# Kernel optimization log

Hardware: AMD Instinct MI355X
Metric: run time of the kernel (lower is better)

The kernel has to match this reference:

```python
import jax, jax.numpy as jnp
import numpy as np

# ---- model hyperparams (match init_kwargs / Mamba1 defaults) ----
SEQ_LEN, PRED_LEN, PATCH, STRIDE = 512, 96, 16, 16
D_MODEL, N_LAYER, N_VARS = 128, 2, 32
D_INNER, D_STATE, D_CONV, DT_RANK = 2 * D_MODEL, 16, 4, 8  # d_inner=2*d_model, dt_rank=ceil(d_model/16)
BATCH = 16
EPS = 1e-5


def setup_inputs() -> dict:
    key = jax.random.key(0)
    ks = jax.random.split(key, 20)
    s = 0.02
    inp = {
        'x_enc': jax.random.normal(ks[0], (BATCH, SEQ_LEN, N_VARS), jnp.float32),
        'x_mark_enc': jax.random.normal(ks[1], (BATCH, SEQ_LEN, 4), jnp.float32),
        'x_dec': jax.random.normal(ks[2], (BATCH, PRED_LEN, N_VARS), jnp.float32),
        'x_mark_dec': jax.random.normal(ks[3], (BATCH, PRED_LEN, 4), jnp.float32),
        # patch embedding: Linear(patch_len -> d_model, bias=False)
        'patch_w': jax.random.normal(ks[4], (D_MODEL, PATCH), jnp.float32) * s,
        # per-layer Mamba1 params, stacked on leading layer axis
        'norm_w': jnp.ones((N_LAYER, D_MODEL), jnp.float32),
        'in_proj_w': jax.random.normal(ks[5], (N_LAYER, 2 * D_INNER, D_MODEL), jnp.float32) * s,
        'conv_w': jax.random.normal(ks[6], (N_LAYER, D_INNER, D_CONV), jnp.float32) * s,
        'conv_b': jnp.zeros((N_LAYER, D_INNER), jnp.float32),
        'x_proj_w': jax.random.normal(ks[7], (N_LAYER, DT_RANK + 2 * D_STATE, D_INNER), jnp.float32) * s,
        'dt_proj_w': jax.random.normal(ks[8], (N_LAYER, D_INNER, DT_RANK), jnp.float32) * s,
        'dt_proj_b': jax.random.normal(ks[9], (N_LAYER, D_INNER), jnp.float32) * 0.1 - 4.0,  # softplus -> small dt
        'A_log': jnp.tile(jnp.log(jnp.arange(1, D_STATE + 1, dtype=jnp.float32))[None, None, :], (N_LAYER, D_INNER, 1)),
        'D_skip': jnp.ones((N_LAYER, D_INNER), jnp.float32),
        'out_proj_w': jax.random.normal(ks[10], (N_LAYER, D_MODEL, D_INNER), jnp.float32) * s,
        'final_norm_w': jnp.ones((D_MODEL,), jnp.float32),
        # head: Linear(d_model*seq_len//patch_len -> pred_len)
        'head_w': jax.random.normal(ks[11], (PRED_LEN, D_MODEL * SEQ_LEN // PATCH), jnp.float32) * s,
        'head_b': jnp.zeros((PRED_LEN,), jnp.float32),
    }
    return inp


def rmsnorm(x, w):
    return x * jax.lax.rsqrt(jnp.mean(x * x, axis=-1, keepdims=True) + EPS) * w


def selective_scan(u, dt, A, Bm, Cm, Dp):
    # u, dt: (B,L,Di); Bm, Cm: (B,L,N); A: (Di,N); Dp: (Di,)
    def step(h, inp):
        dt_t, B_t, C_t, u_t = inp  # (B,Di),(B,N),(B,N),(B,Di)
        dA = jnp.exp(dt_t[:, :, None] * A)                      # (B,Di,N)
        h = dA * h + dt_t[:, :, None] * B_t[:, None, :] * u_t[:, :, None]
        y = jnp.einsum('bdn,bn->bd', h, C_t)
        return h, y

    B_, L, Di = u.shape
    h0 = jnp.zeros((B_, Di, A.shape[1]), u.dtype)
    xs = (dt.transpose(1, 0, 2), Bm.transpose(1, 0, 2), Cm.transpose(1, 0, 2), u.transpose(1, 0, 2))
    _, ys = jax.lax.scan(step, h0, xs)
    return ys.transpose(1, 0, 2) + u * Dp  # skip connection D*u


def mamba_mixer(x, in_w, cw, cb, xp_w, dt_w, dt_b, A_log, Dp, out_w):
    # x: (B,L,d_model)
    xz = x @ in_w.T                                   # (B,L,2*Di)
    xs_, z = jnp.split(xz, 2, axis=-1)
    xc = xs_.transpose(0, 2, 1)                       # (B,Di,L)
    xc = jax.lax.conv_general_dilated(
        xc, cw[:, None, :], (1,), [(D_CONV - 1, 0)],  # causal depthwise conv
        dimension_numbers=('NCH', 'OIH', 'NCH'), feature_group_count=D_INNER)
    xc = jax.nn.silu(xc + cb[None, :, None])
    u = xc.transpose(0, 2, 1)                         # (B,L,Di)
    x_dbl = u @ xp_w.T                                # (B,L,dt_rank+2N)
    dt, Bm, Cm = jnp.split(x_dbl, [DT_RANK, DT_RANK + D_STATE], axis=-1)
    dt = jax.nn.softplus(dt @ dt_w.T + dt_b)          # (B,L,Di)
    A = -jnp.exp(A_log)                               # (Di,N)
    y = selective_scan(u, dt, A, Bm, Cm, Dp)
    y = y * jax.nn.silu(z)
    return y @ out_w.T


def reference(x_enc, x_mark_enc, x_dec, x_mark_dec, patch_w, norm_w, in_proj_w,
              conv_w, conv_b, x_proj_w, dt_proj_w, dt_proj_b, A_log, D_skip,
              out_proj_w, final_norm_w, head_w, head_b):
    b, _, c = x_enc.shape
    # instance norm over time (stats detached)
    means = jax.lax.stop_gradient(jnp.mean(x_enc, axis=1, keepdims=True))
    xe = x_enc - means
    stdev = jax.lax.stop_gradient(jnp.sqrt(jnp.var(xe, axis=1, keepdims=True) + EPS))
    xe = xe / stdev
    # patching: stride == patch_len so unfold == reshape
    xp = xe.transpose(0, 2, 1).reshape(b, c, SEQ_LEN // PATCH, PATCH)  # (b,c,l,patch)
    enc = jnp.einsum('bclp,dp->bcld', xp, patch_w).reshape(b, c * (SEQ_LEN // PATCH), D_MODEL)
    # Mamba encoder: pre-norm residual blocks + final norm
    x = enc
    for i in range(N_LAYER):
        h = rmsnorm(x, norm_w[i])
        x = x + mamba_mixer(h, in_proj_w[i], conv_w[i], conv_b[i], x_proj_w[i],
                            dt_proj_w[i], dt_proj_b[i], A_log[i], D_skip[i], out_proj_w[i])
    x = rmsnorm(x, final_norm_w)
    # prediction head: b (c l) d -> (b c) (l d) -> linear -> (b, pred, c)
    l = SEQ_LEN // PATCH
    xh = x.reshape(b, c, l * D_MODEL)
    out = xh @ head_w.T + head_b                      # (b,c,pred)
    dec_out = out.transpose(0, 2, 1)                  # (b,pred,c)
    dec_out = dec_out * stdev[:, :1, :] + means[:, :1, :]
    return dec_out
```

## Files before the change

### kernel.cpp

```cpp
#include <hip/hip_runtime.h>
#include <hip/hip_bf16.h>
#include <math.h>

#define BATCH   16
#define SEQL    512
#define NVARS   32
#define PATCHL  16
#define LTOK    32
#define DMODEL  128
#define NLAYER  2
#define DIN     256
#define DSTATE  16
#define DTRANK  8
#define DCONV   4
#define PRED    96
#define TOK     1024
#define NTOK    (BATCH*TOK)
#define EPSF    1e-5f
#define NCH     64
#define CHL     16

typedef __attribute__((ext_vector_type(8))) short bf16x8;
typedef __attribute__((ext_vector_type(4))) float f32x4;
typedef __hip_bfloat16 bf16;

__global__ __launch_bounds__(256) void k_cast(
    const float* __restrict__ a, const float* __restrict__ b,
    const float* __restrict__ c, const float* __restrict__ d,
    int na, int nb, int nc, int nd, bf16* __restrict__ out,
    const float* __restrict__ A_log, float* __restrict__ a1s, int* __restrict__ pwf,
    float* __restrict__ hg)
{
    int i = blockIdx.x * 256 + threadIdx.x;
    int total = na + nb + nc + nd;
    if (i < total) {
        float v;
        if (i < na) v = a[i];
        else if (i < na + nb) v = b[i - na];
        else if (i < na + nb + nc) v = c[i - na - nb];
        else v = d[i - na - nb - nc];
        out[i] = __float2bfloat16(v);
    } else if (i < total + NLAYER * DIN) {
        int j = i - total;
        const float* al = A_log + (size_t)j * DSTATE;
        float a1 = -__expf(al[0]);
        bool pw = true;
        #pragma unroll
        for (int n = 1; n < 16; n++) {
            float av = -__expf(al[n]);
            pw = pw && (fabsf(av - (n + 1) * a1) <= 1e-5f * fabsf((n + 1) * a1));
        }
        a1s[j] = a1;
        pwf[j] = pw ? 1 : 0;
    } else if (i < total + NLAYER * DIN + 512 * PRED) {
        hg[i - total - NLAYER * DIN] = 0.f;
    }
}

__global__ __launch_bounds__(256) void k_instnorm_patch(
    const float* __restrict__ x_enc, const float* __restrict__ patch_w,
    const float* __restrict__ nw0,
    float* __restrict__ x, bf16* __restrict__ hbf,
    float* __restrict__ means, float* __restrict__ stdev)
{
    int bc = blockIdx.x;
    int b = bc >> 5, c = bc & 31;
    __shared__ float xe[SEQL];
    __shared__ float pw[DMODEL * PATCHL];
    __shared__ float red[8];
    __shared__ float enc_lds[LTOK][DMODEL];
    int tid = threadIdx.x;

    float v0 = x_enc[((size_t)b * SEQL + tid) * NVARS + c];
    float v1 = x_enc[((size_t)b * SEQL + tid + 256) * NVARS + c];
    for (int i = tid; i < DMODEL * PATCHL; i += 256) pw[i] = patch_w[i];

    float s = v0 + v1;
    for (int o = 1; o < 64; o <<= 1) s += __shfl_xor(s, o, 64);
    if ((tid & 63) == 0) red[tid >> 6] = s;
    __syncthreads();
    float mean = (red[0] + red[1] + red[2] + red[3]) * (1.f / 512.f);

    float d0 = v0 - mean, d1 = v1 - mean;
    float q = d0 * d0 + d1 * d1;
    for (int o = 1; o < 64; o <<= 1) q += __shfl_xor(q, o, 64);
    if ((tid & 63) == 0) red[4 + (tid >> 6)] = q;
    __syncthreads();
    float var = (red[4] + red[5] + red[6] + red[7]) * (1.f / 512.f);
    float sd = sqrtf(var + EPSF);
    float rsd = 1.f / sd;
    if (tid == 0) { means[bc] = mean; stdev[bc] = sd; }

    xe[tid] = d0 * rsd;
    xe[tid + 256] = d1 * rsd;
    __syncthreads();

    size_t base = ((size_t)b * TOK + (size_t)c * LTOK) * DMODEL;
    for (int o = tid; o < LTOK * DMODEL; o += 256) {
        int l = o >> 7, dm = o & 127;
        float acc = 0.f;
        #pragma unroll
        for (int p = 0; p < PATCHL; p++) acc += xe[l * PATCHL + p] * pw[dm * PATCHL + p];
        x[base + o] = acc;
        enc_lds[l][dm] = acc;
    }
    __syncthreads();

    int t = tid >> 3, g = tid & 7;
    float vals[16];
    float ss = 0.f;
    #pragma unroll
    for (int j = 0; j < 16; j++) { vals[j] = enc_lds[t][g * 16 + j]; ss += vals[j] * vals[j]; }
    ss += __shfl_xor(ss, 1, 64);
    ss += __shfl_xor(ss, 2, 64);
    ss += __shfl_xor(ss, 4, 64);
    float rms = rsqrtf(ss * (1.f / DMODEL) + EPSF);
    bf16* hp = hbf + (base + (size_t)t * DMODEL);
    #pragma unroll
    for (int j = 0; j < 16; j++)
        hp[g * 16 + j] = __float2bfloat16(vals[j] * rms * nw0[g * 16 + j]);
}

template <int MODE>
__global__ __launch_bounds__(256) void mfma_gemm(
    const bf16* __restrict__ A, const bf16* __restrict__ W,
    float* __restrict__ C, bf16* __restrict__ C2, bf16* __restrict__ C3,
    int M, int N, int K, int lda, int kper)
{
    __shared__ ushort Asm[128][40];
    __shared__ ushort Wsm[128][40];
    int bm = blockIdx.y * 128, bn = blockIdx.x * 128;
    int tid = threadIdx.x;
    int w = tid >> 6, l = tid & 63;
    int wr = w >> 1, wc = w & 1;
    int kb = (l >> 4) * 8, lr = l & 15;

    f32x4 acc[4][4];
    #pragma unroll
    for (int i = 0; i < 4; i++)
        #pragma unroll
        for (int j = 0; j < 4; j++) acc[i][j] = (f32x4){0.f, 0.f, 0.f, 0.f};

    int kbeg = blockIdx.z * kper;
    for (int k0 = kbeg; k0 < kbeg + kper; k0 += 32) {
        #pragma unroll
        for (int i = 0; i < 2; i++) {
            int idx = tid + 256 * i;
            int row = idx >> 2, kq = (idx & 3) * 8;
            *(float4*)&Asm[row][kq] =
                *(const float4*)&A[(size_t)(bm + row) * lda + k0 + kq];
            float4 wv = make_float4(0.f, 0.f, 0.f, 0.f);
            if (bn + row < N)
                wv = *(const float4*)&W[(size_t)(bn + row) * K + k0 + kq];
            *(float4*)&Wsm[row][kq] = wv;
        }
        __syncthreads();
        bf16x8 af[4], bfr[4];
        #pragma unroll
        for (int f = 0; f < 4; f++) {
            af[f]  = *(const bf16x8*)&Asm[wr * 64 + f * 16 + lr][kb];
            bfr[f] = *(const bf16x8*)&Wsm[wc * 64 + f * 16 + lr][kb];
        }
        #pragma unroll
        for (int mf = 0; mf < 4; mf++)
            #pragma unroll
            for (int nf = 0; nf < 4; nf++)
                acc[mf][nf] = __builtin_amdgcn_mfma_f32_16x16x32_bf16(
                    af[mf], bfr[nf], acc[mf][nf], 0, 0, 0);
        __syncthreads();
    }

    int rbase = bm + wr * 64 + (l >> 4) * 4;
    int cbase = bn + wc * 64 + lr;
    #pragma unroll
    for (int mf = 0; mf < 4; mf++) {
        #pragma unroll
        for (int nf = 0; nf < 4; nf++) {
            int n = cbase + nf * 16;
            if (n >= N) continue;
            #pragma unroll
            for (int r = 0; r < 4; r++) {
                int m = rbase + mf * 16 + r;
                float v = acc[mf][nf][r];
                if (MODE == 2) atomicAdd(&C[(size_t)m * N + n], v);
                else {
                    if (n < 256) C3[(size_t)m * 256 + n] = __float2bfloat16(v);
                    else C2[(size_t)m * 256 + (n - 256)] = __float2bfloat16(v);
                }
            }
        }
    }
}

__device__ __forceinline__ float softplus_f(float x) {
    return (x > 8.f) ? x : __logf(1.f + __expf(x));
}

__global__ __launch_bounds__(256) void k_convx1(
    const bf16* __restrict__ xs, const float* __restrict__ cw,
    const float* __restrict__ cb, const bf16* __restrict__ xw,
    const float* __restrict__ dtw, const float* __restrict__ dtb_,
    const float* __restrict__ a1s, const int* __restrict__ pwf,
    const float* __restrict__ A_log,
    bf16* __restrict__ ubf, float* __restrict__ xdbl,
    bf16* __restrict__ q, float* __restrict__ sdt_out)
{
    int blk = blockIdx.x;
    int b = blk >> 6, ch = blk & (NCH - 1);
    int d = threadIdx.x;
    __shared__ ushort u_lds[16][264];
    __shared__ float xdbl_lds[16][40];

    float c0 = cw[d * 4], c1 = cw[d * 4 + 1], c2 = cw[d * 4 + 2], c3 = cw[d * 4 + 3];
    float cbias = cb[d];
    int tloc0 = ch * CHL;
    const bf16* col = xs + ((size_t)b * TOK + tloc0) * 256 + d;
    float xv[19];
    #pragma unroll
    for (int i = 0; i < 19; i++) {
        int tg = tloc0 - 3 + i;
        xv[i] = (tg >= 0) ? __bfloat162float(col[(size_t)(i - 3) * 256]) : 0.f;
    }
    bf16* uout = ubf + ((size_t)b * TOK + tloc0) * 256 + d;
    #pragma unroll
    for (int t = 0; t < 16; t++) {
        float a = cbias + xv[t] * c0 + xv[t + 1] * c1 + xv[t + 2] * c2 + xv[t + 3] * c3;
        float s = __fdividef(a, 1.f + __expf(-a));
        bf16 ub = __float2bfloat16(s);
        u_lds[t][d] = *(ushort*)&ub;
        uout[(size_t)t * 256] = ub;
    }
    __syncthreads();

    int w = d >> 6, l = d & 63;
    if (w < 3) {
        int lr = l & 15, kb = (l >> 4) * 8;
        int nrow = w * 16 + lr;
        bool valid = nrow < 40;
        const bf16* wrow = xw + (size_t)nrow * 256;
        f32x4 acc = (f32x4){0.f, 0.f, 0.f, 0.f};
        #pragma unroll
        for (int ks = 0; ks < 8; ks++) {
            bf16x8 af = *(const bf16x8*)&u_lds[lr][ks * 32 + kb];
            bf16x8 bfr = (bf16x8){0, 0, 0, 0, 0, 0, 0, 0};
            if (valid) bfr = *(const bf16x8*)&wrow[ks * 32 + kb];
            acc = __builtin_amdgcn_mfma_f32_16x16x32_bf16(af, bfr, acc, 0, 0, 0);
        }
        int ncol = w * 16 + (l & 15);
        if (ncol < 40) {
            #pragma unroll
            for (int r = 0; r < 4; r++) {
                int t = (l >> 4) * 4 + r;
                xdbl_lds[t][ncol] = acc[r];
                xdbl[((size_t)b * TOK + tloc0 + t) * 40 + ncol] = acc[r];
            }
        }
    }
    __syncthreads();

    float a1 = a1s[d];
    bool pw = pwf[d] != 0;
    float w8[8];
    #pragma unroll
    for (int j = 0; j < 8; j++) w8[j] = dtw[d * 8 + j];
    float bias = dtb_[d];
    float h[16];
    #pragma unroll
    for (int n = 0; n < 16; n++) h[n] = 0.f;
    float sdt = 0.f;

    if (pw) {
        for (int t = 0; t < CHL; t++) {
            float acc = bias;
            #pragma unroll
            for (int j = 0; j < 8; j++) acc += xdbl_lds[t][j] * w8[j];
            float dtv = softplus_f(acc);
            ushort uraw = u_lds[t][d];
            float uu = __bfloat162float(*(bf16*)&uraw);
            sdt += dtv;
            float du = dtv * uu;
            float dA[16];
            dA[0] = __expf(dtv * a1);
            #pragma unroll
            for (int n = 1; n < 16; n++) dA[n] = dA[(n - 1) >> 1] * dA[n >> 1];
            #pragma unroll
            for (int n = 0; n < 16; n++)
                h[n] = dA[n] * h[n] + du * xdbl_lds[t][8 + n];
        }
    } else {
        float Av[16];
        #pragma unroll
        for (int n = 0; n < 16; n++) Av[n] = -__expf(A_log[d * 16 + n]);
        for (int t = 0; t < CHL; t++) {
            float acc = bias;
            #pragma unroll
            for (int j = 0; j < 8; j++) acc += xdbl_lds[t][j] * w8[j];
            float dtv = softplus_f(acc);
            ushort uraw = u_lds[t][d];
            float uu = __bfloat162float(*(bf16*)&uraw);
            sdt += dtv;
            float du = dtv * uu;
            #pragma unroll
            for (int n = 0; n < 16; n++)
                h[n] = __expf(dtv * Av[n]) * h[n] + du * xdbl_lds[t][8 + n];
        }
    }
    bf16* qp = q + ((size_t)blk * 16) * 256 + d;
    #pragma unroll
    for (int n = 0; n < 16; n++) qp[(size_t)n * 256] = __float2bfloat16(h[n]);
    sdt_out[(size_t)blk * 256 + d] = sdt;
}

__global__ __launch_bounds__(256) void k_scan2(
    const float* __restrict__ A_log, const float* __restrict__ sdt_in,
    bf16* __restrict__ q)
{
    int idx = blockIdx.x * 256 + threadIdx.x;
    int d = idx & 255, n = (idx >> 8) & 15, b = idx >> 12;
    float Av = -__expf(A_log[d * 16 + n]);
    float h = 0.f;
    for (int g = 0; g < NCH / 8; g++) {
        float qv[8], sv[8];
        #pragma unroll
        for (int j = 0; j < 8; j++) {
            size_t blk = (size_t)b * NCH + g * 8 + j;
            qv[j] = __bfloat162float(q[(blk * 16 + n) * 256 + d]);
            sv[j] = sdt_in[blk * 256 + d];
        }
        #pragma unroll
        for (int j = 0; j < 8; j++) {
            size_t blk = (size_t)b * NCH + g * 8 + j;
            float P = __expf(Av * sv[j]);
            q[(blk * 16 + n) * 256 + d] = __float2bfloat16(h);
            h = P * h + qv[j];
        }
    }
}

__global__ __launch_bounds__(256) void k_scan3o(
    const bf16* __restrict__ ubf, const float* __restrict__ xdbl,
    const float* __restrict__ dtw, const float* __restrict__ dtb_,
    const float* __restrict__ a1s, const int* __restrict__ pwf,
    const float* __restrict__ A_log, const float* __restrict__ Dp,
    const bf16* __restrict__ q, const bf16* __restrict__ zbf,
    const bf16* __restrict__ ow, const float* __restrict__ nwn,
    float* __restrict__ x, bf16* __restrict__ hout)
{
    int blk = blockIdx.x;
    int b = blk >> 6, ch = blk & (NCH - 1);
    int d = threadIdx.x;
    __shared__ ushort y_lds[16][264];
    __shared__ float xn_lds[16][132];

    float a1 = a1s[d];
    bool pw = pwf[d] != 0;
    float w8[8];
    #pragma unroll
    for (int j = 0; j < 8; j++) w8[j] = dtw[d * 8 + j];
    float bias = dtb_[d];
    float Dv = Dp[d];
    float h[16];
    const bf16* qp = q + ((size_t)blk * 16) * 256 + d;
    #pragma unroll
    for (int n = 0; n < 16; n++) h[n] = __bfloat162float(qp[(size_t)n * 256]);

    size_t tok0 = (size_t)b * TOK + ch * CHL;
    const float* row = xdbl + tok0 * 40;
    const bf16* up = ubf + tok0 * 256 + d;
    const bf16* zp = zbf + tok0 * 256 + d;

    if (pw) {
        for (int t = 0; t < CHL; t++, row += 40, up += 256, zp += 256) {
            float acc = bias;
            #pragma unroll
            for (int j = 0; j < 8; j++) acc += row[j] * w8[j];
            float dtv = softplus_f(acc);
            float uu = __bfloat162float(*up);
            float du = dtv * uu;
            float dA[16];
            dA[0] = __expf(dtv * a1);
            #pragma unroll
            for (int n = 1; n < 16; n++) dA[n] = dA[(n - 1) >> 1] * dA[n >> 1];
            float ya = 0.f;
            #pragma unroll
            for (int n = 0; n < 16; n++) {
                h[n] = dA[n] * h[n] + du * row[8 + n];
                ya += h[n] * row[24 + n];
            }
            float zv = __bfloat162float(*zp);
            float sz = __fdividef(zv, 1.f + __expf(-zv));
            bf16 yb = __float2bfloat16((ya + uu * Dv) * sz);
            y_lds[t][d] = *(ushort*)&yb;
        }
    } else {
        float Av[16];
        #pragma unroll
        for (int n = 0; n < 16; n++) Av[n] = -__expf(A_log[d * 16 + n]);
        for (int t = 0; t < CHL; t++, row += 40, up += 256, zp += 256) {
            float acc = bias;
            #pragma unroll
            for (int j = 0; j < 8; j++) acc += row[j] * w8[j];
            float dtv = softplus_f(acc);
            float uu = __bfloat162float(*up);
            float du = dtv * uu;
            float ya = 0.f;
            #pragma unroll
            for (int n = 0; n < 16; n++) {
                h[n] = __expf(dtv * Av[n]) * h[n] + du * row[8 + n];
                ya += h[n] * row[24 + n];
            }
            float zv = __bfloat162float(*zp);
            float sz = __fdividef(zv, 1.f + __expf(-zv));
            bf16 yb = __float2bfloat16((ya + uu * Dv) * sz);
            y_lds[t][d] = *(ushort*)&yb;
        }
    }
    __syncthreads();

    int w = d >> 6, l = d & 63;
    int lr = l & 15, kb = (l >> 4) * 8;
    const bf16* wr0 = ow + (size_t)(w * 32 + lr) * 256;
    const bf16* wr1 = ow + (size_t)(w * 32 + 16 + lr) * 256;
    f32x4 acc0 = (f32x4){0.f, 0.f, 0.f, 0.f};
    f32x4 acc1 = (f32x4){0.f, 0.f, 0.f, 0.f};
    #pragma unroll
    for (int ks = 0; ks < 8; ks++) {
        bf16x8 af = *(const bf16x8*)&y_lds[lr][ks * 32 + kb];
        bf16x8 b0 = *(const bf16x8*)&wr0[ks * 32 + kb];
        bf16x8 b1 = *(const bf16x8*)&wr1[ks * 32 + kb];
        acc0 = __builtin_amdgcn_mfma_f32_16x16x32_bf16(af, b0, acc0, 0, 0, 0);
        acc1 = __builtin_amdgcn_mfma_f32_16x16x32_bf16(af, b1, acc1, 0, 0, 0);
    }
    int trow = (l >> 4) * 4;
    float* xp = x + (tok0 + trow) * (size_t)DMODEL;
    #pragma unroll
    for (int r = 0; r < 4; r++) {
        float v0 = xp[(size_t)r * DMODEL + w * 32 + lr] + acc0[r];
        float v1 = xp[(size_t)r * DMODEL + w * 32 + 16 + lr] + acc1[r];
        xp[(size_t)r * DMODEL + w * 32 + lr] = v0;
        xp[(size_t)r * DMODEL + w * 32 + 16 + lr] = v1;
        xn_lds[trow + r][w * 32 + lr] = v0;
        xn_lds[trow + r][w * 32 + 16 + lr] = v1;
    }
    __syncthreads();

    int t = d >> 4, g = d & 15;
    float vals[8];
    float ss = 0.f;
    #pragma unroll
    for (int j = 0; j < 8; j++) { vals[j] = xn_lds[t][g * 8 + j]; ss += vals[j] * vals[j]; }
    ss += __shfl_xor(ss, 1, 64);
    ss += __shfl_xor(ss, 2, 64);
    ss += __shfl_xor(ss, 4, 64);
    ss += __shfl_xor(ss, 8, 64);
    float rms = rsqrtf(ss * (1.f / DMODEL) + EPSF);
    bf16* hp = hout + (tok0 + t) * (size_t)DMODEL;
    #pragma unroll
    for (int j = 0; j < 8; j++)
        hp[g * 8 + j] = __float2bfloat16(vals[j] * rms * nwn[g * 8 + j]);
}

__global__ __launch_bounds__(256) void k_head_ep(
    const float* __restrict__ hg, const float* __restrict__ hb,
    const float* __restrict__ means, const float* __restrict__ stdev,
    float* __restrict__ out)
{
    int i = blockIdx.x * 256 + threadIdx.x;
    if (i >= BATCH * PRED * NVARS) return;
    int c = i & 31;
    int p = (i >> 5) % PRED;
    int b = i / (PRED * NVARS);
    float v = hg[((size_t)b * NVARS + c) * PRED + p] + hb[p];
    out[i] = v * stdev[b * NVARS + c] + means[b * NVARS + c];
}

extern "C" void kernel_launch(void* const* d_in, const int* in_sizes, int n_in,
                              void* d_out, int out_size, void* d_ws, size_t ws_size,
                              hipStream_t stream)
{
    const float* x_enc   = (const float*)d_in[0];
    const float* patch_w = (const float*)d_in[4];
    const float* norm_w  = (const float*)d_in[5];
    const float* in_w    = (const float*)d_in[6];
    const float* conv_w  = (const float*)d_in[7];
    const float* conv_b  = (const float*)d_in[8];
    const float* xp_w    = (const float*)d_in[9];
    const float* dt_w    = (const float*)d_in[10];
    const float* dt_b    = (const float*)d_in[11];
    const float* A_log   = (const float*)d_in[12];
    const float* D_skip  = (const float*)d_in[13];
    const float* out_w   = (const float*)d_in[14];
    const float* fnorm_w = (const float*)d_in[15];
    const float* head_w  = (const float*)d_in[16];
    const float* head_b  = (const float*)d_in[17];
    float* out = (float*)d_out;

    float* ws    = (float*)d_ws;
    float* means = ws;
    float* stdv  = ws + 512;
    float* x     = ws + 1024;
    float* xdbl  = x    + (size_t)NTOK * 128;
    float* sbuf  = xdbl + (size_t)NTOK * 40;
    float* hg    = sbuf + (size_t)BATCH * NCH * DIN;
    float* a1s   = hg + 512 * PRED;
    int*   pwf   = (int*)(a1s + NLAYER * DIN);
    bf16* hbf  = (bf16*)(pwf + NLAYER * DIN);
    bf16* xsbf = hbf + (size_t)NTOK * 128;
    bf16* zbf  = xsbf + (size_t)NTOK * 256;
    bf16* ubf  = zbf + (size_t)NTOK * 256;
    bf16* qbuf = ubf + (size_t)NTOK * 256;
    bf16* wbf  = qbuf + (size_t)BATCH * NCH * DSTATE * DIN;

    const int NIW = NLAYER * 2 * DIN * DMODEL;
    const int NXW = NLAYER * (DTRANK + 2*DSTATE) * DIN;
    const int NOW = NLAYER * DMODEL * DIN;
    const int NHW = PRED * LTOK * DMODEL;
    bf16* iwbf = wbf;
    bf16* xwbf = iwbf + NIW;
    bf16* owbf = xwbf + NXW;
    bf16* hwbf = owbf + NOW;

    int castN = NIW + NXW + NOW + NHW + NLAYER * DIN + 512 * PRED;
    k_cast<<<(castN + 255) / 256, 256, 0, stream>>>(
        in_w, xp_w, out_w, head_w, NIW, NXW, NOW, NHW, wbf, A_log, a1s, pwf, hg);

    k_instnorm_patch<<<BATCH * NVARS, 256, 0, stream>>>(
        x_enc, patch_w, norm_w, x, hbf, means, stdv);

    for (int layer = 0; layer < NLAYER; layer++) {
        const float* cw  = conv_w + layer * DIN * DCONV;
        const float* cb  = conv_b + layer * DIN;
        const float* dw  = dt_w   + layer * DIN * DTRANK;
        const float* db  = dt_b   + layer * DIN;
        const float* al  = A_log  + layer * DIN * DSTATE;
        const float* dp  = D_skip + layer * DIN;
        const float* a1l = a1s + layer * DIN;
        const int*   pwl = pwf + layer * DIN;
        const bf16* iw = iwbf + (size_t)layer * 2 * DIN * DMODEL;
        const bf16* xw = xwbf + (size_t)layer * (DTRANK + 2 * DSTATE) * DIN;
        const bf16* ow = owbf + (size_t)layer * DMODEL * DIN;
        const float* nwn = (layer + 1 < NLAYER) ? (norm_w + (layer + 1) * DMODEL) : fnorm_w;

        mfma_gemm<3><<<dim3(4, NTOK / 128, 1), 256, 0, stream>>>(
            hbf, iw, nullptr, zbf, xsbf, NTOK, 512, DMODEL, DMODEL, DMODEL);
        k_convx1<<<BATCH * NCH, 256, 0, stream>>>(
            xsbf, cw, cb, xw, dw, db, a1l, pwl, al, ubf, xdbl, qbuf, sbuf);
        k_scan2<<<(BATCH * DIN * DSTATE) / 256, 256, 0, stream>>>(al, sbuf, qbuf);
        k_scan3o<<<BATCH * NCH, 256, 0, stream>>>(
            ubf, xdbl, dw, db, a1l, pwl, al, dp, qbuf, zbf, ow, nwn, x, hbf);
    }

    mfma_gemm<2><<<dim3(1, 4, 32), 256, 0, stream>>>(
        hbf, hwbf, hg, nullptr, nullptr, 512, PRED, LTOK * DMODEL, LTOK * DMODEL, 128);
    k_head_ep<<<(BATCH * PRED * NVARS + 255) / 256, 256, 0, stream>>>(
        hg, head_b, means, stdv, out);
}
```

Measured before the change: 156.4 us.

## Fuse in_proj GEMM into conv and scan-output kernels

Removes the standalone in_proj GEMM per layer. The x-half projection is now computed inside k_convx1 over a 32-token window, the last 16 tokens of the previous chunk supplying the conv halo. The z-half is computed inside k_scan3o from hbf before hbf is overwritten. This drops two bf16 NTOK×256 intermediate buffers and one launch per layer, at the cost of recomputing halo rows, extra LDS, and weight loads repeated per block from global or L2.

After: 155.0 us. Within noise of the previous version (-0.9%).

```diff
diff --git a/kernel.cpp b/kernel.cpp
--- a/kernel.cpp
+++ b/kernel.cpp
@@ -121,11 +121,9 @@
         hp[g * 16 + j] = __float2bfloat16(vals[j] * rms * nw0[g * 16 + j]);
 }
 
-template <int MODE>
-__global__ __launch_bounds__(256) void mfma_gemm(
+__global__ __launch_bounds__(256) void mfma_gemm_at(
     const bf16* __restrict__ A, const bf16* __restrict__ W,
-    float* __restrict__ C, bf16* __restrict__ C2, bf16* __restrict__ C3,
-    int M, int N, int K, int lda, int kper)
+    float* __restrict__ C, int M, int N, int K, int kper)
 {
     __shared__ ushort Asm[128][40];
     __shared__ ushort Wsm[128][40];
@@ -148,7 +146,7 @@
             int idx = tid + 256 * i;
             int row = idx >> 2, kq = (idx & 3) * 8;
             *(float4*)&Asm[row][kq] =
-                *(const float4*)&A[(size_t)(bm + row) * lda + k0 + kq];
+                *(const float4*)&A[(size_t)(bm + row) * K + k0 + kq];
             float4 wv = make_float4(0.f, 0.f, 0.f, 0.f);
             if (bn + row < N)
                 wv = *(const float4*)&W[(size_t)(bn + row) * K + k0 + kq];
@@ -179,15 +177,8 @@
             int n = cbase + nf * 16;
             if (n >= N) continue;
             #pragma unroll
-            for (int r = 0; r < 4; r++) {
-                int m = rbase + mf * 16 + r;
-                float v = acc[mf][nf][r];
-                if (MODE == 2) atomicAdd(&C[(size_t)m * N + n], v);
-                else {
-                    if (n < 256) C3[(size_t)m * 256 + n] = __float2bfloat16(v);
-                    else C2[(size_t)m * 256 + (n - 256)] = __float2bfloat16(v);
-                }
-            }
+            for (int r = 0; r < 4; r++)
+                atomicAdd(&C[(size_t)(rbase + mf * 16 + r) * N + n], acc[mf][nf][r]);
         }
     }
 }
@@ -197,8 +188,9 @@
 }
 
 __global__ __launch_bounds__(256) void k_convx1(
-    const bf16* __restrict__ xs, const float* __restrict__ cw,
-    const float* __restrict__ cb, const bf16* __restrict__ xw,
+    const bf16* __restrict__ hbf, const bf16* __restrict__ iwA,
+    const float* __restrict__ cw, const float* __restrict__ cb,
+    const bf16* __restrict__ xw,
     const float* __restrict__ dtw, const float* __restrict__ dtb_,
     const float* __restrict__ a1s, const int* __restrict__ pwf,
     const float* __restrict__ A_log,
@@ -208,18 +200,69 @@
     int blk = blockIdx.x;
     int b = blk >> 6, ch = blk & (NCH - 1);
     int d = threadIdx.x;
+    __shared__ ushort hb_lds[32][136];
+    __shared__ ushort xs_lds[32][264];
     __shared__ ushort u_lds[16][264];
     __shared__ float xdbl_lds[16][40];
 
+    int tloc0 = ch * CHL;
+
+    {
+        int r = d >> 3, c8 = (d & 7) * 16;
+        int tl = tloc0 - 16 + r;
+        float4 v0 = make_float4(0.f, 0.f, 0.f, 0.f), v1 = v0;
+        if (tl >= 0) {
+            const bf16* src = hbf + ((size_t)b * TOK + tl) * DMODEL + c8;
+            v0 = *(const float4*)src;
+            v1 = *(const float4*)(src + 8);
+        }
+        *(float4*)&hb_lds[r][c8] = v0;
+        *(float4*)&hb_lds[r][c8 + 8] = v1;
+    }
+    __syncthreads();
+
+    {
+        int w = d >> 6, l = d & 63;
+        int lr = l & 15, kb = (l >> 4) * 8;
+        f32x4 accx[2][4];
+        #pragma unroll
+        for (int mf = 0; mf < 2; mf++)
+            #pragma unroll
+            for (int nf = 0; nf < 4; nf++) accx[mf][nf] = (f32x4){0.f, 0.f, 0.f, 0.f};
+        #pragma unroll
+        for (int ks = 0; ks < 4; ks++) {
+            bf16x8 af0 = *(const bf16x8*)&hb_lds[lr][ks * 32 + kb];
+            bf16x8 af1 = *(const bf16x8*)&hb_lds[16 + lr][ks * 32 + kb];
+            #pragma unroll
+            for (int nf = 0; nf < 4; nf++) {
+                const bf16* wrow = iwA + (size_t)(w * 64 + nf * 16 + lr) * DMODEL;
+                bf16x8 bfr = *(const bf16x8*)&wrow[ks * 32 + kb];
+                accx[0][nf] = __builtin_amdgcn_mfma_f32_16x16x32_bf16(af0, bfr, accx[0][nf], 0, 0, 0);
+                accx[1][nf] = __builtin_amdgcn_mfma_f32_16x16x32_bf16(af1, bfr, accx[1][nf], 0, 0, 0);
+            }
+        }
+        #pragma unroll
+        for (int mf = 0; mf < 2; mf++)
+            #pragma unroll
+            for (int nf = 0; nf < 4; nf++) {
+                int ncol = w * 64 + nf * 16 + lr;
+                #pragma unroll
+                for (int r = 0; r < 4; r++) {
+                    int row = mf * 16 + (l >> 4) * 4 + r;
+                    bf16 xb = __float2bfloat16(accx[mf][nf][r]);
+                    xs_lds[row][ncol] = *(ushort*)&xb;
+                }
+            }
+    }
+    __syncthreads();
+
     float c0 = cw[d * 4], c1 = cw[d * 4 + 1], c2 = cw[d * 4 + 2], c3 = cw[d * 4 + 3];
     float cbias = cb[d];
-    int tloc0 = ch * CHL;
-    const bf16* col = xs + ((size_t)b * TOK + tloc0) * 256 + d;
     float xv[19];
     #pragma unroll
     for (int i = 0; i < 19; i++) {
-        int tg = tloc0 - 3 + i;
-        xv[i] = (tg >= 0) ? __bfloat162float(col[(size_t)(i - 3) * 256]) : 0.f;
+        ushort raw = xs_lds[13 + i][d];
+        xv[i] = __bfloat162float(*(bf16*)&raw);
     }
     bf16* uout = ubf + ((size_t)b * TOK + tloc0) * 256 + d;
     #pragma unroll
@@ -232,27 +275,29 @@
     }
     __syncthreads();
 
-    int w = d >> 6, l = d & 63;
-    if (w < 3) {
-        int lr = l & 15, kb = (l >> 4) * 8;
-        int nrow = w * 16 + lr;
-        bool valid = nrow < 40;
-        const bf16* wrow = xw + (size_t)nrow * 256;
-        f32x4 acc = (f32x4){0.f, 0.f, 0.f, 0.f};
-        #pragma unroll
-        for (int ks = 0; ks < 8; ks++) {
-            bf16x8 af = *(const bf16x8*)&u_lds[lr][ks * 32 + kb];
-            bf16x8 bfr = (bf16x8){0, 0, 0, 0, 0, 0, 0, 0};
-            if (valid) bfr = *(const bf16x8*)&wrow[ks * 32 + kb];
-            acc = __builtin_amdgcn_mfma_f32_16x16x32_bf16(af, bfr, acc, 0, 0, 0);
-        }
-        int ncol = w * 16 + (l & 15);
-        if (ncol < 40) {
-            #pragma unroll
-            for (int r = 0; r < 4; r++) {
-                int t = (l >> 4) * 4 + r;
-                xdbl_lds[t][ncol] = acc[r];
-                xdbl[((size_t)b * TOK + tloc0 + t) * 40 + ncol] = acc[r];
+    {
+        int w = d >> 6, l = d & 63;
+        if (w < 3) {
+            int lr = l & 15, kb = (l >> 4) * 8;
+            int nrow = w * 16 + lr;
+            bool valid = nrow < 40;
+            const bf16* wrow = xw + (size_t)nrow * 256;
+            f32x4 acc = (f32x4){0.f, 0.f, 0.f, 0.f};
+            #pragma unroll
+            for (int ks = 0; ks < 8; ks++) {
+                bf16x8 af = *(const bf16x8*)&u_lds[lr][ks * 32 + kb];
+                bf16x8 bfr = (bf16x8){0, 0, 0, 0, 0, 0, 0, 0};
+                if (valid) bfr = *(const bf16x8*)&wrow[ks * 32 + kb];
+                acc = __builtin_amdgcn_mfma_f32_16x16x32_bf16(af, bfr, acc, 0, 0, 0);
+            }
+            int ncol = w * 16 + (l & 15);
+            if (ncol < 40) {
+                #pragma unroll
+                for (int r = 0; r < 4; r++) {
+                    int t = (l >> 4) * 4 + r;
+                    xdbl_lds[t][ncol] = acc[r];
+                    xdbl[((size_t)b * TOK + tloc0 + t) * 40 + ncol] = acc[r];
+                }
             }
         }
     }
@@ -339,18 +384,57 @@
 
 __global__ __launch_bounds__(256) void k_scan3o(
     const bf16* __restrict__ ubf, const float* __restrict__ xdbl,
+    const bf16* __restrict__ iwZ,
     const float* __restrict__ dtw, const float* __restrict__ dtb_,
     const float* __restrict__ a1s, const int* __restrict__ pwf,
     const float* __restrict__ A_log, const float* __restrict__ Dp,
-    const bf16* __restrict__ q, const bf16* __restrict__ zbf,
-    const bf16* __restrict__ ow, const float* __restrict__ nwn,
-    float* __restrict__ x, bf16* __restrict__ hout)
+    const bf16* __restrict__ q, const bf16* __restrict__ ow,
+    const float* __restrict__ nwn,
+    float* __restrict__ x, bf16* __restrict__ hbf)
 {
     int blk = blockIdx.x;
     int b = blk >> 6, ch = blk & (NCH - 1);
     int d = threadIdx.x;
+    __shared__ ushort hz_lds[16][136];
+    __shared__ ushort z_lds[16][264];
     __shared__ ushort y_lds[16][264];
     __shared__ float xn_lds[16][132];
+
+    size_t tok0 = (size_t)b * TOK + ch * CHL;
+
+    {
+        int r = d >> 4, c8 = (d & 15) * 8;
+        *(float4*)&hz_lds[r][c8] = *(const float4*)(hbf + (tok0 + r) * DMODEL + c8);
+    }
+    __syncthreads();
+
+    {
+        int w = d >> 6, l = d & 63;
+        int lr = l & 15, kb = (l >> 4) * 8;
+        f32x4 accz[4];
+        #pragma unroll
+        for (int nf = 0; nf < 4; nf++) accz[nf] = (f32x4){0.f, 0.f, 0.f, 0.f};
+        #pragma unroll
+        for (int ks = 0; ks < 4; ks++) {
+            bf16x8 af = *(const bf16x8*)&hz_lds[lr][ks * 32 + kb];
+            #pragma unroll
+            for (int nf = 0; nf < 4; nf++) {
+                const bf16* wrow = iwZ + (size_t)(w * 64 + nf * 16 + lr) * DMODEL;
+                bf16x8 bfr = *(const bf16x8*)&wrow[ks * 32 + kb];
+                accz[nf] = __builtin_amdgcn_mfma_f32_16x16x32_bf16(af, bfr, accz[nf], 0, 0, 0);
+            }
+        }
+        #pragma unroll
+        for (int nf = 0; nf < 4; nf++) {
+            int ncol = w * 64 + nf * 16 + lr;
+            #pragma unroll
+            for (int r = 0; r < 4; r++) {
+                bf16 zb = __float2bfloat16(accz[nf][r]);
+                z_lds[(l >> 4) * 4 + r][ncol] = *(ushort*)&zb;
+            }
+        }
+    }
+    __syncthreads();
 
     float a1 = a1s[d];
     bool pw = pwf[d] != 0;
@@ -364,13 +448,11 @@
     #pragma unroll
     for (int n = 0; n < 16; n++) h[n] = __bfloat162float(qp[(size_t)n * 256]);
 
-    size_t tok0 = (size_t)b * TOK + ch * CHL;
     const float* row = xdbl + tok0 * 40;
     const bf16* up = ubf + tok0 * 256 + d;
-    const bf16* zp = zbf + tok0 * 256 + d;
 
     if (pw) {
-        for (int t = 0; t < CHL; t++, row += 40, up += 256, zp += 256) {
+        for (int t = 0; t < CHL; t++, row += 40, up += 256) {
             float acc = bias;
             #pragma unroll
             for (int j = 0; j < 8; j++) acc += row[j] * w8[j];
@@ -387,7 +469,8 @@
                 h[n] = dA[n] * h[n] + du * row[8 + n];
                 ya += h[n] * row[24 + n];
             }
-            float zv = __bfloat162float(*zp);
+            ushort zraw = z_lds[t][d];
+            float zv = __bfloat162float(*(bf16*)&zraw);
             float sz = __fdividef(zv, 1.f + __expf(-zv));
             bf16 yb = __float2bfloat16((ya + uu * Dv) * sz);
             y_lds[t][d] = *(ushort*)&yb;
@@ -396,7 +479,7 @@
         float Av[16];
         #pragma unroll
         for (int n = 0; n < 16; n++) Av[n] = -__expf(A_log[d * 16 + n]);
-        for (int t = 0; t < CHL; t++, row += 40, up += 256, zp += 256) {
+        for (int t = 0; t < CHL; t++, row += 40, up += 256) {
             float acc = bias;
             #pragma unroll
             for (int j = 0; j < 8; j++) acc += row[j] * w8[j];
@@ -409,7 +492,8 @@
                 h[n] = __expf(dtv * Av[n]) * h[n] + du * row[8 + n];
                 ya += h[n] * row[24 + n];
             }
-            float zv = __bfloat162float(*zp);
+            ushort zraw = z_lds[t][d];
+            float zv = __bfloat162float(*(bf16*)&zraw);
             float sz = __fdividef(zv, 1.f + __expf(-zv));
             bf16 yb = __float2bfloat16((ya + uu * Dv) * sz);
             y_lds[t][d] = *(ushort*)&yb;
@@ -454,7 +538,7 @@
     ss += __shfl_xor(ss, 4, 64);
     ss += __shfl_xor(ss, 8, 64);
     float rms = rsqrtf(ss * (1.f / DMODEL) + EPSF);
-    bf16* hp = hout + (tok0 + t) * (size_t)DMODEL;
+    bf16* hp = hbf + (tok0 + t) * (size_t)DMODEL;
     #pragma unroll
     for (int j = 0; j < 8; j++)
         hp[g * 8 + j] = __float2bfloat16(vals[j] * rms * nwn[g * 8 + j]);
@@ -505,9 +589,7 @@
     float* a1s   = hg + 512 * PRED;
     int*   pwf   = (int*)(a1s + NLAYER * DIN);
     bf16* hbf  = (bf16*)(pwf + NLAYER * DIN);
-    bf16* xsbf = hbf + (size_t)NTOK * 128;
-    bf16* zbf  = xsbf + (size_t)NTOK * 256;
-    bf16* ubf  = zbf + (size_t)NTOK * 256;
+    bf16* ubf  = hbf + (size_t)NTOK * 128;
     bf16* qbuf = ubf + (size_t)NTOK * 256;
     bf16* wbf  = qbuf + (size_t)BATCH * NCH * DSTATE * DIN;
 
@@ -536,22 +618,21 @@
         const float* dp  = D_skip + layer * DIN;
         const float* a1l = a1s + layer * DIN;
         const int*   pwl = pwf + layer * DIN;
-        const bf16* iw = iwbf + (size_t)layer * 2 * DIN * DMODEL;
+        const bf16* iwA = iwbf + (size_t)layer * 2 * DIN * DMODEL;
+        const bf16* iwZ = iwA + (size_t)DIN * DMODEL;
         const bf16* xw = xwbf + (size_t)layer * (DTRANK + 2 * DSTATE) * DIN;
         const bf16* ow = owbf + (size_t)layer * DMODEL * DIN;
         const float* nwn = (layer + 1 < NLAYER) ? (norm_w + (layer + 1) * DMODEL) : fnorm_w;
 
-        mfma_gemm<3><<<dim3(4, NTOK / 128, 1), 256, 0, stream>>>(
-            hbf, iw, nullptr, zbf, xsbf, NTOK, 512, DMODEL, DMODEL, DMODEL);
         k_convx1<<<BATCH * NCH, 256, 0, stream>>>(
-            xsbf, cw, cb, xw, dw, db, a1l, pwl, al, ubf, xdbl, qbuf, sbuf);
+            hbf, iwA, cw, cb, xw, dw, db, a1l, pwl, al, ubf, xdbl, qbuf, sbuf);
         k_scan2<<<(BATCH * DIN * DSTATE) / 256, 256, 0, stream>>>(al, sbuf, qbuf);
         k_scan3o<<<BATCH * NCH, 256, 0, stream>>>(
-            ubf, xdbl, dw, db, a1l, pwl, al, dp, qbuf, zbf, ow, nwn, x, hbf);
-    }
-
-    mfma_gemm<2><<<dim3(1, 4, 32), 256, 0, stream>>>(
-        hbf, hwbf, hg, nullptr, nullptr, 512, PRED, LTOK * DMODEL, LTOK * DMODEL, 128);
+            ubf, xdbl, iwZ, dw, db, a1l, pwl, al, dp, qbuf, ow, nwn, x, hbf);
+    }
+
+    mfma_gemm_at<<<dim3(1, 4, 32), 256, 0, stream>>>(
+        hbf, hwbf, hg, 512, PRED, LTOK * DMODEL, 128);
     k_head_ep<<<(BATCH * PRED * NVARS + 255) / 256, 256, 0, stream>>>(
         hg, head_b, means, stdv, out);
 }
```
